# Kernel optimization log

Hardware: AMD Instinct MI355X
Metric: run time of the kernel (lower is better)

## Reference

```python
import jax, jax.numpy as jnp
import numpy as np
from jax import lax

B, N, C = 16, 1024, 768
HID = 128           # route_hidden_dim (Cattn bottleneck + router hidden)
OUT = 2304          # qkv out_feature


def setup_inputs() -> dict:
    key = jax.random.key(0)
    ks = jax.random.split(key, 16)
    s = 0.02
    return {
        "input":  jax.random.normal(ks[0], (B, N, C), jnp.float32),
        "H": 32,
        "W": 32,
        "input2": jax.random.normal(ks[1], (B, N, C), jnp.float32),
        # qkv linear
        "qkv_w": jax.random.normal(ks[2], (OUT, C), jnp.float32) * s,
        "qkv_b": jax.random.normal(ks[3], (OUT,), jnp.float32) * s,
        # Cattn (vida_refine): fc1 -> dwconv -> gelu -> fc2
        "fc1_w": jax.random.normal(ks[4], (HID, C), jnp.float32) * s,
        "fc1_b": jnp.zeros((HID,), jnp.float32),
        "dw_w":  jax.random.normal(ks[5], (HID, 1, 3, 3), jnp.float32) * np.sqrt(2.0 / 9.0),
        "dw_b":  jnp.zeros((HID,), jnp.float32),
        "fc2_w": jax.random.normal(ks[6], (C, HID), jnp.float32) * s,
        "fc2_b": jnp.zeros((C,), jnp.float32),
        # router MLP: 1 -> HID -> 2
        "r1_w": jax.random.normal(ks[7], (HID, 1), jnp.float32) * s,
        "r1_b": jnp.zeros((HID,), jnp.float32),
        "r2_w": jax.random.normal(ks[8], (2, HID), jnp.float32) * s,
        "r2_b": jnp.zeros((2,), jnp.float32),
    }


def _linear(x, w, b):
    return jnp.einsum("bnc,oc->bno", x, w) + b


def _cattn(x, H, W, fc1_w, fc1_b, dw_w, dw_b, fc2_w, fc2_b):
    # fc1 -> depthwise 3x3 conv over HxW -> GELU(exact) -> fc2
    x = _linear(x, fc1_w, fc1_b)                       # [B,N,HID]
    b, n, h = x.shape
    xi = x.transpose(0, 2, 1).reshape(b, h, H, W)      # [B,HID,H,W]
    xi = lax.conv_general_dilated(
        xi, dw_w, window_strides=(1, 1), padding="SAME",
        feature_group_count=h,
        dimension_numbers=("NCHW", "OIHW", "NCHW"),
    ) + dw_b[None, :, None, None]
    x = xi.reshape(b, h, n).transpose(0, 2, 1)         # [B,N,HID]
    x = jax.nn.gelu(x, approximate=False)              # torch nn.GELU default = erf
    return _linear(x, fc2_w, fc2_b)                    # [B,N,C]


def _get_logit(inp, refine_x2):
    # cosine sim between per-batch token-mean of `inp` and refine_x2, then
    # per-batch min-max normalization (skipped when max == min)
    mean = jnp.mean(inp, axis=1, keepdims=True)        # [B,1,C]
    dot = jnp.sum(refine_x2 * mean, axis=-1, keepdims=True)
    n1 = jnp.linalg.norm(mean, axis=-1, keepdims=True)
    n2 = jnp.linalg.norm(refine_x2, axis=-1, keepdims=True)
    csim = dot / (n1 * n2)                             # [B,N,1]
    mn = jnp.min(csim, axis=1, keepdims=True)
    mx = jnp.max(csim, axis=1, keepdims=True)
    rng = mx - mn
    return jnp.where(rng != 0, (csim - mn) / jnp.where(rng != 0, rng, 1.0), csim)


def reference(input, H, W, input2, qkv_w, qkv_b, fc1_w, fc1_b, dw_w, dw_b,
              fc2_w, fc2_b, r1_w, r1_b, r2_w, r2_b):
    q1 = _linear(input, qkv_w, qkv_b)                              # [B,N,OUT]
    refine_x2 = input2 + _cattn(input2, H, W, fc1_w, fc1_b, dw_w, dw_b, fc2_w, fc2_b)
    q2 = _linear(refine_x2, qkv_w, qkv_b)                          # [B,N,OUT]
    csim = _get_logit(input, refine_x2)                            # [B,N,1]
    h = jax.nn.relu(_linear(csim, r1_w, r1_b))                     # [B,N,HID]
    logits = jax.nn.sigmoid(_linear(h, r2_w, r2_b))                # [B,N,2]
    # gumbel_softmax(hard=False, tau=1) with a fixed key for determinism
    g = jax.random.gumbel(jax.random.key(42), logits.shape, logits.dtype)
    router = jax.nn.softmax(logits + g, axis=-1)[:, :, 0]          # [B,N]
    return (q1, q2, router)
```

## Files before the change

kernel.cpp:

```cpp
#include <hip/hip_runtime.h>
#include <cstdint>
#include <cstddef>

#define BQ 16
#define NT 1024
#define CH 768
#define HIDN 128
#define OUTF 2304
#define MTOT (BQ*NT)

typedef __attribute__((ext_vector_type(4))) float f32x4;
typedef __attribute__((ext_vector_type(8))) short short8;

__device__ __forceinline__ unsigned short f2bf(float f){
  unsigned u = __float_as_uint(f);
  u += 0x7FFFu + ((u >> 16) & 1u);
  return (unsigned short)(u >> 16);
}
__device__ __forceinline__ float bf2f(unsigned short h){
  return __uint_as_float(((unsigned)h) << 16);
}

__device__ __forceinline__ void gload16(const void* g, void* l){
  __builtin_amdgcn_global_load_lds((const __attribute__((address_space(1))) void*)g,
                                   (__attribute__((address_space(3))) void*)l, 16, 0, 0);
}

__device__ __forceinline__ void mfma16(f32x4& d, short8 a, short8 b){
  asm volatile("v_mfma_f32_16x16x32_bf16 %0, %1, %2, %0" : "+v"(d) : "v"(a), "v"(b));
}

__global__ void k_f2bf_all(const float* __restrict__ in0, const float* __restrict__ in1,
                           const float* __restrict__ in2, const float* __restrict__ in3,
                           const float* __restrict__ in4,
                           unsigned short* __restrict__ o0, unsigned short* __restrict__ o1,
                           unsigned short* __restrict__ o2, unsigned short* __restrict__ o3,
                           unsigned short* __restrict__ o4)
{
  const long step = (long)2048 * 256 * 4;
  for (long i = (long)(blockIdx.x * 256 + threadIdx.x) * 4; i < 27131904L; i += step){
    const float* s; unsigned short* d; long off;
    if      (i < 12582912L){ s = in0; d = o0; off = i; }
    else if (i < 25165824L){ s = in1; d = o1; off = i - 12582912L; }
    else if (i < 26935296L){ s = in2; d = o2; off = i - 25165824L; }
    else if (i < 27033600L){ s = in3; d = o3; off = i - 26935296L; }
    else                   { s = in4; d = o4; off = i - 27033600L; }
    float4 v = *reinterpret_cast<const float4*>(s + off);
    ushort4 o;
    o.x = f2bf(v.x); o.y = f2bf(v.y); o.z = f2bf(v.z); o.w = f2bf(v.w);
    *reinterpret_cast<ushort4*>(d + off) = o;
  }
}

#define STAGE(matB_, buf_, h_, t_) { \
    const unsigned short* g_ = ((matB_) ? Bbase : Abase) + (size_t)(h_)*128*K + (size_t)(t_)*64; \
    char* d_ = ldsWaveDst + (matB_)*65536 + (buf_)*32768 + (h_)*16384; \
    gload16(g_, d_); \
    gload16(g_ + rowK64, d_ + 8192); \
  }

#define PH_OPEN() \
    asm volatile("s_barrier" ::: "memory"); \
    asm volatile("s_waitcnt lgkmcnt(0)" ::: "memory"); \
    __builtin_amdgcn_sched_barrier(0); \
    __builtin_amdgcn_s_setprio(1);

#define PH_CLOSE() \
    __builtin_amdgcn_s_setprio(0); \
    asm volatile("s_barrier" ::: "memory");

#define MF16(mb, nb, BV) \
    _Pragma("unroll") \
    for (int ks = 0; ks < 2; ++ks) \
      _Pragma("unroll") \
      for (int mf = 0; mf < 4; ++mf) \
        _Pragma("unroll") \
        for (int nf = 0; nf < 2; ++nf) \
          mfma16(acc[(mb)+mf][(nb)+nf], av[mf][ks], BV[nf][ks]);

#define TILE(t_, b_) { \
    const int t = (t_); const int b = (b_); \
    _Pragma("unroll") for (int mf = 0; mf < 4; ++mf){ av[mf][0]=ldA(b,mf,0); av[mf][1]=ldA(b,mf,1); } \
    _Pragma("unroll") for (int nf = 0; nf < 2; ++nf){ b0v[nf][0]=ldB(b,nf,0); b0v[nf][1]=ldB(b,nf,1); } \
    if (t+1 < T) STAGE(0, b^1, 1, t+1); \
    PH_OPEN(); MF16(0,0,b0v); PH_CLOSE(); \
    _Pragma("unroll") for (int nf = 0; nf < 2; ++nf){ b1v[nf][0]=ldB(b,2+nf,0); b1v[nf][1]=ldB(b,2+nf,1); } \
    if (t+1 < T) STAGE(1, b^1, 0, t+1); \
    PH_OPEN(); MF16(0,2,b1v); PH_CLOSE(); \
    _Pragma("unroll") for (int mf = 0; mf < 4; ++mf){ av[mf][0]=ldA(b,4+mf,0); av[mf][1]=ldA(b,4+mf,1); } \
    if (t+2 < T) STAGE(0, b, 0, t+2); \
    PH_OPEN(); MF16(4,2,b1v); PH_CLOSE(); \
    if (t+2 < T) STAGE(1, b, 1, t+2); \
    PH_OPEN(); MF16(4,0,b0v); \
    __builtin_amdgcn_s_setprio(0); \
    if (t+2 < T) { asm volatile("s_waitcnt vmcnt(4)" ::: "memory"); } \
    else         { asm volatile("s_waitcnt vmcnt(0)" ::: "memory"); } \
    asm volatile("s_barrier" ::: "memory"); \
  }

template<int T>
__device__ __forceinline__
void gemm256_body(char* lds8,
                  const unsigned short* __restrict__ A,
                  const unsigned short* __restrict__ B,
                  const float* __restrict__ bias,
                  float* __restrict__ C,
                  int N, int K, int nbn, int bid, int nwg)
{
  const int tid = threadIdx.x;
  const int ln = tid & 63, wv = tid >> 6;
  const int wm = wv >> 2, wn = wv & 3;
  const int llo = ln & 15, lhi = ln >> 4;

  const int cpx = nwg >> 3;
  const int swz = (bid & 7) * cpx + (bid >> 3);
  const int bm = swz / nbn, bn = swz % nbn;
  const int m0 = bm * 256, n0 = bn * 256;

  const int srow = tid >> 3;
  const int sslot = (tid & 7) ^ (srow & 7);
  const unsigned short* Abase = A + (size_t)(m0 + srow) * K + sslot * 8;
  const unsigned short* Bbase = B + (size_t)(n0 + srow) * K + sslot * 8;
  const size_t rowK64 = (size_t)64 * K;
  char* ldsWaveDst = lds8 + (wv << 10);

  const int swz0 = ((lhi ^ (ln & 7)) << 4);
  const char* aRd0 = lds8 + (wm*64 + llo)*128 + swz0;
  const char* aRd1 = lds8 + (wm*64 + llo)*128 + (swz0 ^ 64);
  const char* bRd0 = lds8 + 65536 + (wn*32 + llo)*128 + swz0;
  const char* bRd1 = lds8 + 65536 + (wn*32 + llo)*128 + (swz0 ^ 64);

  auto ldA = [&](int b, int mf, int ks) -> short8 {
    const char* p = (ks ? aRd1 : aRd0) + b*32768 + (mf>>2)*16384 + (mf&3)*2048;
    return *reinterpret_cast<const short8*>(p);
  };
  auto ldB = [&](int b, int nf, int ks) -> short8 {
    const char* p = (ks ? bRd1 : bRd0) + b*32768 + (nf>>1)*16384 + (nf&1)*2048;
    return *reinterpret_cast<const short8*>(p);
  };

  f32x4 acc[8][4];
  #pragma unroll
  for (int m = 0; m < 8; ++m)
    #pragma unroll
    for (int n = 0; n < 4; ++n) acc[m][n] = 0.0f;

  STAGE(0, 0, 0, 0);
  STAGE(1, 0, 1, 0);
  STAGE(0, 0, 1, 0);
  STAGE(1, 0, 0, 0);
  STAGE(0, 1, 0, 1);
  STAGE(1, 1, 1, 1);
  asm volatile("s_waitcnt vmcnt(4)" ::: "memory");
  asm volatile("s_barrier" ::: "memory");

  short8 av[4][2], b0v[2][2], b1v[2][2];
  #pragma unroll 1
  for (int t0 = 0; t0 < T; t0 += 2){
    TILE(t0,   0);
    TILE(t0+1, 1);
  }

  asm volatile("s_nop 7\n\ts_nop 7\n\ts_nop 7" ::: );

  #pragma unroll
  for (int mf = 0; mf < 8; ++mf){
    const int row = m0 + (mf>>2)*128 + wm*64 + (mf&3)*16 + lhi*4;
    #pragma unroll
    for (int j = 0; j < 4; ++j){
      #pragma unroll
      for (int nf = 0; nf < 4; ++nf){
        const int col = n0 + (nf>>1)*128 + wn*32 + (nf&1)*16 + llo;
        C[(size_t)(row + j) * N + col] = acc[mf][nf][j] + bias[col];
      }
    }
  }
}

__device__ __forceinline__
void fc1_body(char* lds, const unsigned short* __restrict__ A,
              const unsigned short* __restrict__ B,
              const float* __restrict__ bias, unsigned short* __restrict__ Cb, int fb)
{
  const int tid = threadIdx.x;
  if (tid >= 256){
    #pragma unroll 1
    for (int i = 0; i < 24; ++i){ __syncthreads(); __syncthreads(); }
    return;
  }
  unsigned short (*sA)[32] = (unsigned short(*)[32])lds;
  unsigned short (*sB)[32] = (unsigned short(*)[32])(lds + 8192);
  const int wv = tid >> 6, ln = tid & 63;
  const int wr = wv >> 1, wc = wv & 1;
  const int lhi = ln >> 4, llo = ln & 15;
  const int m0 = fb * 128, n0 = 0;
  const int N = 128, K = 768;

  f32x4 acc[4][4];
  #pragma unroll
  for (int m = 0; m < 4; ++m)
    #pragma unroll
    for (int n = 0; n < 4; ++n) acc[m][n] = 0.0f;

  const int lrow = ln >> 2;
  const int lk8  = (ln & 3) * 8;

  #pragma unroll 1
  for (int kt = 0; kt < 768; kt += 32){
    #pragma unroll
    for (int cc = 0; cc < 2; ++cc){
      int c = wv * 2 + cc;
      gload16(A + (size_t)(m0 + c*16 + lrow) * K + kt + lk8, &sA[c*16][0]);
      gload16(B + (size_t)(n0 + c*16 + lrow) * K + kt + lk8, &sB[c*16][0]);
    }
    __syncthreads();

    short8 av[4], bv[4];
    #pragma unroll
    for (int m = 0; m < 4; ++m)
      av[m] = *reinterpret_cast<const short8*>(&sA[wr*64 + m*16 + llo][lhi*8]);
    #pragma unroll
    for (int n = 0; n < 4; ++n)
      bv[n] = *reinterpret_cast<const short8*>(&sB[wc*64 + n*16 + llo][lhi*8]);

    #pragma unroll
    for (int m = 0; m < 4; ++m)
      #pragma unroll
      for (int n = 0; n < 4; ++n)
        mfma16(acc[m][n], bv[n], av[m]);
    __syncthreads();
  }

  asm volatile("s_nop 7\n\ts_nop 7\n\ts_nop 7" ::: );

  float4 bias4[4];
  #pragma unroll
  for (int n = 0; n < 4; ++n)
    bias4[n] = *reinterpret_cast<const float4*>(&bias[n0 + wc*64 + n*16 + lhi*4]);

  #pragma unroll
  for (int m = 0; m < 4; ++m){
    const int row = m0 + wr*64 + m*16 + llo;
    #pragma unroll
    for (int n = 0; n < 4; ++n){
      const int colbase = n0 + wc*64 + n*16 + lhi*4;
      ushort4 o;
      o.x = f2bf(acc[m][n][0] + bias4[n].x);
      o.y = f2bf(acc[m][n][1] + bias4[n].y);
      o.z = f2bf(acc[m][n][2] + bias4[n].z);
      o.w = f2bf(acc[m][n][3] + bias4[n].w);
      *reinterpret_cast<ushort4*>(&Cb[(size_t)row * N + colbase]) = o;
    }
  }
}

__device__ __forceinline__
void mean_body(char* lds, const unsigned short* __restrict__ x1b,
               float* __restrict__ meanb, float* __restrict__ n1p, int mbid)
{
  float (*tmp)[128] = (float(*)[128])lds;
  const int b = mbid / 6, cg = mbid % 6;
  const int tid = threadIdx.x;
  const int oct = tid & 15, rg = tid >> 4;
  const unsigned short* ip = x1b + (size_t)b*NT*CH + (size_t)rg*32*CH + cg*128 + oct*8;

  float s[8];
  #pragma unroll
  for (int j = 0; j < 8; ++j) s[j] = 0.f;
  #pragma unroll 4
  for (int r = 0; r < 32; ++r){
    short8 v = *reinterpret_cast<const short8*>(ip + (size_t)r*CH);
    #pragma unroll
    for (int j = 0; j < 8; ++j) s[j] += bf2f((unsigned short)v[j]);
  }
  #pragma unroll
  for (int j = 0; j < 8; ++j) tmp[rg][oct*8 + j] = s[j];
  __syncthreads();

  if (tid < 128){
    float m = 0.f;
    #pragma unroll
    for (int g = 0; g < 32; ++g) m += tmp[g][tid];
    m *= (1.0f/1024.0f);
    meanb[b*CH + cg*128 + tid] = m;
    float q = m * m;
    for (int off = 32; off; off >>= 1) q += __shfl_down(q, off, 64);
    if ((tid & 63) == 0) n1p[b*12 + cg*2 + (tid >> 6)] = q;
  }
}

__global__ __launch_bounds__(512, 2)
void k_combo(const unsigned short* __restrict__ x1b, const unsigned short* __restrict__ wqb,
             const float* __restrict__ qkv_b, float* __restrict__ q1,
             const unsigned short* __restrict__ xrb, const unsigned short* __restrict__ w1b,
             const float* __restrict__ fc1_b, unsigned short* __restrict__ t1dst,
             float* __restrict__ meanb, float* __restrict__ n1p)
{
  __shared__ __align__(1024) char lds8[131072];
  const int bid = blockIdx.x;
  if (bid < 576){
    gemm256_body<CH/64>(lds8, x1b, wqb, qkv_b, q1, OUTF, CH, OUTF/256, bid, 576);
  } else if (bid < 704){
    fc1_body(lds8, xrb, w1b, fc1_b, t1dst, bid - 576);
  } else {
    mean_body(lds8, x1b, meanb, n1p, bid - 704);
  }
}

template<int T>
__global__ __launch_bounds__(512, 2)
void k_gemm256(const unsigned short* __restrict__ A,
               const unsigned short* __restrict__ B,
               const float* __restrict__ bias,
               float* __restrict__ C,
               int N, int K, int nbn)
{
  __shared__ __align__(1024) char lds8[131072];
  gemm256_body<T>(lds8, A, B, bias, C, N, K, nbn, blockIdx.x, gridDim.x);
}

template<int EPI>
__global__ __launch_bounds__(256, 2)
void k_gemm(const unsigned short* __restrict__ A, const unsigned short* __restrict__ B,
            const float* __restrict__ bias, const unsigned short* __restrict__ addb,
            unsigned short* __restrict__ Cb,
            const float* __restrict__ meanb, float* __restrict__ part,
            int M, int N, int K)
{
  __shared__ unsigned short sA[128][32];
  __shared__ unsigned short sB[128][32];
  const int tid = threadIdx.x;
  const int wv = tid >> 6, ln = tid & 63;
  const int wr = wv >> 1, wc = wv & 1;
  const int lhi = ln >> 4, llo = ln & 15;
  const int m0 = blockIdx.x * 128, n0 = blockIdx.y * 128;

  f32x4 acc[4][4];
  #pragma unroll
  for (int m = 0; m < 4; ++m)
    #pragma unroll
    for (int n = 0; n < 4; ++n) acc[m][n] = 0.0f;

  const int lrow = ln >> 2;
  const int lk8  = (ln & 3) * 8;

  for (int kt = 0; kt < K; kt += 32){
    #pragma unroll
    for (int cc = 0; cc < 2; ++cc){
      int c = wv * 2 + cc;
      gload16(A + (size_t)(m0 + c*16 + lrow) * K + kt + lk8, &sA[c*16][0]);
      gload16(B + (size_t)(n0 + c*16 + lrow) * K + kt + lk8, &sB[c*16][0]);
    }
    __syncthreads();

    short8 av[4], bv[4];
    #pragma unroll
    for (int m = 0; m < 4; ++m)
      av[m] = *reinterpret_cast<const short8*>(&sA[wr*64 + m*16 + llo][lhi*8]);
    #pragma unroll
    for (int n = 0; n < 4; ++n)
      bv[n] = *reinterpret_cast<const short8*>(&sB[wc*64 + n*16 + llo][lhi*8]);

    #pragma unroll
    for (int m = 0; m < 4; ++m)
      #pragma unroll
      for (int n = 0; n < 4; ++n)
        mfma16(acc[m][n], bv[n], av[m]);
    __syncthreads();
  }

  asm volatile("s_nop 7\n\ts_nop 7\n\ts_nop 7" ::: );

  float4 bias4[4];
  #pragma unroll
  for (int n = 0; n < 4; ++n)
    bias4[n] = *reinterpret_cast<const float4*>(&bias[n0 + wc*64 + n*16 + lhi*4]);

  {
    const int bb = m0 >> 10;
    const float* mp = meanb + bb * CH;
    float4 mp4[4];
    #pragma unroll
    for (int n = 0; n < 4; ++n)
      mp4[n] = *reinterpret_cast<const float4*>(&mp[n0 + wc*64 + n*16 + lhi*4]);

    #pragma unroll
    for (int m = 0; m < 4; ++m){
      const int row = m0 + wr*64 + m*16 + llo;
      float dsum = 0.f, qsum = 0.f;
      #pragma unroll
      for (int n = 0; n < 4; ++n){
        const int colbase = n0 + wc*64 + n*16 + lhi*4;
        ushort4 a4 = *reinterpret_cast<const ushort4*>(&addb[(size_t)row * N + colbase]);
        float v0 = acc[m][n][0] + bias4[n].x + bf2f(a4.x);
        float v1 = acc[m][n][1] + bias4[n].y + bf2f(a4.y);
        float v2 = acc[m][n][2] + bias4[n].z + bf2f(a4.z);
        float v3 = acc[m][n][3] + bias4[n].w + bf2f(a4.w);
        ushort4 o; o.x = f2bf(v0); o.y = f2bf(v1); o.z = f2bf(v2); o.w = f2bf(v3);
        *reinterpret_cast<ushort4*>(&Cb[(size_t)row * N + colbase]) = o;
        dsum += v0*mp4[n].x + v1*mp4[n].y + v2*mp4[n].z + v3*mp4[n].w;
        qsum += v0*v0 + v1*v1 + v2*v2 + v3*v3;
      }
      dsum += __shfl_xor(dsum, 16, 64);  qsum += __shfl_xor(qsum, 16, 64);
      dsum += __shfl_xor(dsum, 32, 64);  qsum += __shfl_xor(qsum, 32, 64);
      if (ln < 16){
        const int slot = blockIdx.y * 2 + wc;
        part[(size_t)slot * MTOT + row] = dsum;
        part[(size_t)(12 + slot) * MTOT + row] = qsum;
      }
    }
  }
}

__global__ void k_dwgelu(const unsigned short* __restrict__ t1b, const float* __restrict__ dww,
                         const float* __restrict__ dwb, unsigned short* __restrict__ t2)
{
  int idx = blockIdx.x * blockDim.x + threadIdx.x;
  int hq = idx & 31; int t = idx >> 5;
  int h = hq * 4;
  int n = t & (NT-1); int b = t >> 10;
  int y = n >> 5, x = n & 31;

  float w[4][9];
  #pragma unroll
  for (int i = 0; i < 4; ++i)
    #pragma unroll
    for (int k = 0; k < 9; ++k) w[i][k] = dww[(h+i)*9 + k];

  float a0 = dwb[h+0], a1 = dwb[h+1], a2 = dwb[h+2], a3 = dwb[h+3];
  #pragma unroll
  for (int dy = -1; dy <= 1; ++dy){
    int yy = y + dy; if ((unsigned)yy >= 32u) continue;
    #pragma unroll
    for (int dx = -1; dx <= 1; ++dx){
      int xx = x + dx; if ((unsigned)xx >= 32u) continue;
      ushort4 v = *reinterpret_cast<const ushort4*>(&t1b[((size_t)b*NT + yy*32 + xx)*HIDN + h]);
      int k = (dy+1)*3 + (dx+1);
      a0 += bf2f(v.x) * w[0][k]; a1 += bf2f(v.y) * w[1][k];
      a2 += bf2f(v.z) * w[2][k]; a3 += bf2f(v.w) * w[3][k];
    }
  }
  const float is2 = 0.70710678118654752440f;
  a0 = 0.5f*a0*(1.0f + erff(a0*is2));
  a1 = 0.5f*a1*(1.0f + erff(a1*is2));
  a2 = 0.5f*a2*(1.0f + erff(a2*is2));
  a3 = 0.5f*a3*(1.0f + erff(a3*is2));
  ushort4 o; o.x = f2bf(a0); o.y = f2bf(a1); o.z = f2bf(a2); o.w = f2bf(a3);
  *reinterpret_cast<ushort4*>(&t2[(size_t)t*HIDN + h]) = o;
}

__device__ __forceinline__ void threefry(unsigned k0, unsigned k1, unsigned x0, unsigned x1,
                                         unsigned& o0, unsigned& o1){
  unsigned ks2 = k0 ^ k1 ^ 0x1BD11BDAu;
  x0 += k0; x1 += k1;
#define TFR(r) { x0 += x1; x1 = (x1 << r) | (x1 >> (32 - r)); x1 ^= x0; }
  TFR(13) TFR(15) TFR(26) TFR(6)  x0 += k1;  x1 += ks2 + 1u;
  TFR(17) TFR(29) TFR(16) TFR(24) x0 += ks2; x1 += k0 + 2u;
  TFR(13) TFR(15) TFR(26) TFR(6)  x0 += k0;  x1 += k1 + 3u;
  TFR(17) TFR(29) TFR(16) TFR(24) x0 += k1;  x1 += ks2 + 4u;
  TFR(13) TFR(15) TFR(26) TFR(6)  x0 += ks2; x1 += k0 + 5u;
#undef TFR
  o0 = x0; o1 = x1;
}

__device__ __forceinline__ float gumbel_from_bits(unsigned bits){
  float f = __uint_as_float((bits >> 9) | 0x3F800000u) - 1.0f;
  const float TINY = 1.17549435e-38f;
  float u = fmaxf(TINY, f + TINY);
  return -logf(-logf(u));
}

__global__ void k_router(const float* __restrict__ part, const float* __restrict__ n1p,
                         const float* __restrict__ r1w, const float* __restrict__ r1b,
                         const float* __restrict__ r2w, const float* __restrict__ r2b,
                         float* __restrict__ out)
{
  int b = blockIdx.x, tid = threadIdx.x;
  __shared__ float cs[NT];
  __shared__ float red[8];
  __shared__ float w1s[HIDN], b1s[HIDN], w20s[HIDN], w21s[HIDN];
  if (tid < HIDN){
    w1s[tid]  = r1w[tid];
    b1s[tid]  = r1b[tid];
    w20s[tid] = r2w[tid];
    w21s[tid] = r2w[HIDN + tid];
  }
  float n1s = 0.f;
  #pragma unroll
  for (int s = 0; s < 12; ++s) n1s += n1p[b*12 + s];
  float n1 = sqrtf(n1s);
  float lmin = 3.4e38f, lmax = -3.4e38f;
  #pragma unroll
  for (int j = 0; j < 4; ++j){
    int tk = tid + j*256;
    int t = b*NT + tk;
    float dot = 0.f, q = 0.f;
    #pragma unroll
    for (int s = 0; s < 12; ++s){
      dot += part[(size_t)s * MTOT + t];
      q   += part[(size_t)(12 + s) * MTOT + t];
    }
    float v = dot / (n1 * sqrtf(q));
    cs[tk] = v;
    lmin = fminf(lmin, v); lmax = fmaxf(lmax, v);
  }
  int ln = tid & 63, wv = tid >> 6;
  for (int off = 32; off; off >>= 1){
    lmin = fminf(lmin, __shfl_down(lmin, off, 64));
    lmax = fmaxf(lmax, __shfl_down(lmax, off, 64));
  }
  if (ln == 0){ red[wv] = lmin; red[4+wv] = lmax; }
  __syncthreads();
  float mn = fminf(fminf(red[0], red[1]), fminf(red[2], red[3]));
  float mx = fmaxf(fmaxf(red[4], red[5]), fmaxf(red[6], red[7]));
  float rng = mx - mn;
  bool nz = (rng != 0.0f);

  const float r2b0 = r2b[0], r2b1 = r2b[1];
  float v[4], l0[4], l1[4];
  #pragma unroll
  for (int j = 0; j < 4; ++j){
    float c0 = cs[tid + j*256];
    v[j] = nz ? (c0 - mn) / rng : c0;
    l0[j] = r2b0; l1[j] = r2b1;
  }
  for (int k = 0; k < HIDN; ++k){
    float a = w1s[k], bb = b1s[k], c0 = w20s[k], c1 = w21s[k];
    #pragma unroll
    for (int j = 0; j < 4; ++j){
      float hh = fmaxf(v[j] * a + bb, 0.f);
      l0[j] += hh * c0;
      l1[j] += hh * c1;
    }
  }
  #pragma unroll
  for (int j = 0; j < 4; ++j){
    float s0 = 1.f / (1.f + expf(-l0[j]));
    float s1 = 1.f / (1.f + expf(-l1[j]));
    int t = b*NT + tid + j*256;
    unsigned o0, o1;
    threefry(0u, 42u, 0u, (unsigned)(2*t),     o0, o1);
    float g0 = gumbel_from_bits(o0 ^ o1);
    threefry(0u, 42u, 0u, (unsigned)(2*t + 1), o0, o1);
    float g1 = gumbel_from_bits(o0 ^ o1);
    out[t] = 1.f / (1.f + expf((s1 + g1) - (s0 + g0)));
  }
}

extern "C" void kernel_launch(void* const* d_in, const int* in_sizes, int n_in,
                              void* d_out, int out_size, void* d_ws, size_t ws_size,
                              hipStream_t stream)
{
  (void)in_sizes; (void)n_in; (void)out_size;
  const float* input  = (const float*)d_in[0];
  const float* input2 = (const float*)d_in[3];
  const float* qkv_w  = (const float*)d_in[4];
  const float* qkv_b  = (const float*)d_in[5];
  const float* fc1_w  = (const float*)d_in[6];
  const float* fc1_b  = (const float*)d_in[7];
  const float* dw_w   = (const float*)d_in[8];
  const float* dw_b   = (const float*)d_in[9];
  const float* fc2_w  = (const float*)d_in[10];
  const float* fc2_b  = (const float*)d_in[11];
  const float* r1_w   = (const float*)d_in[12];
  const float* r1_b   = (const float*)d_in[13];
  const float* r2_w   = (const float*)d_in[14];
  const float* r2_b   = (const float*)d_in[15];

  float* q1 = (float*)d_out;
  float* q2 = q1 + (size_t)MTOT * OUTF;
  float* router = q1 + (size_t)2 * MTOT * OUTF;

  if (ws_size < 67000000u) return;

  char* ws = (char*)d_ws;
  unsigned short* x1b = (unsigned short*)ws; ws += (size_t)MTOT*CH*2;
  unsigned short* xrb = (unsigned short*)ws; ws += (size_t)MTOT*CH*2;
  unsigned short* wqb = (unsigned short*)ws; ws += (size_t)OUTF*CH*2;
  unsigned short* w1b = (unsigned short*)ws; ws += (size_t)HIDN*CH*2;
  unsigned short* w2b = (unsigned short*)ws; ws += (size_t)CH*HIDN*2;
  unsigned short* t1b = (unsigned short*)ws; ws += (size_t)MTOT*HIDN*4;
  unsigned short* t2  = (unsigned short*)ws; ws += (size_t)MTOT*HIDN*2;
  float*          mb  = (float*)ws;          ws += (size_t)BQ*CH*4;
  float*          n1p = (float*)ws;          ws += 1024;
  float*          part= (float*)t1b;

  k_f2bf_all<<<dim3(2048), 256, 0, stream>>>(
      input, input2, qkv_w, fc1_w, fc2_w, x1b, xrb, wqb, w1b, w2b);

  unsigned short* t1dst = t1b + (size_t)MTOT*HIDN;
  k_combo<<<dim3(800), 512, 0, stream>>>(
      x1b, wqb, qkv_b, q1, xrb, w1b, fc1_b, t1dst, mb, n1p);

  k_dwgelu<<<dim3(MTOT*32/256), 256, 0, stream>>>(t1dst, dw_w, dw_b, t2);

  k_gemm<1><<<dim3(MTOT/128, CH/128), 256, 0, stream>>>(
      t2, w2b, fc2_b, xrb, xrb, mb, part, MTOT, CH, HIDN);

  k_gemm256<CH/64><<<dim3(576), 512, 0, stream>>>(
      xrb, wqb, qkv_b, q2, OUTF, CH, OUTF/256);

  k_router<<<dim3(BQ), 256, 0, stream>>>(part, n1p, r1_w, r1_b, r2_w, r2_b, router);
}
```

Measured before the change: 242.8 us.

## Fold fc2 into q2 GEMM via precomputed Wq·W2 and concatenated K

Rewrites q2 = (x2 + G·W2ᵀ + b2)·Wqᵀ + bq as x2·Wqᵀ + G·(Wq·W2)ᵀ + (bq + Wq·b2). The fused weight and bias are computed in a prep kernel and extra k_combo blocks. The q2 GEMM then runs over a concatenated K of 768+128, and the fc2/cosine-similarity partials are computed in the same launch. This removes the serial dependency of q2 on materializing refine_x2 in bf16 and drops one launch. In exchange it adds about 17% more MFMA work to the q2 GEMM and a serial, poorly coalesced bias-fold kernel, and rounding now differs slightly from the reference order.

```diff
diff --git a/kernel.cpp b/kernel.cpp
--- a/kernel.cpp
+++ b/kernel.cpp
@@ -52,11 +52,41 @@
   }
 }
 
+__global__ void k_prep(const float* __restrict__ qkv_w, const float* __restrict__ qkv_b,
+                       const float* __restrict__ fc2_w, const float* __restrict__ fc2_b,
+                       float* __restrict__ qb2, unsigned short* __restrict__ w2tb,
+                       float* __restrict__ z128)
+{
+  const int bid = blockIdx.x, tid = threadIdx.x;
+  if (bid < 9){
+    __shared__ float fb[CH];
+    for (int i = tid; i < CH; i += 256) fb[i] = fc2_b[i];
+    __syncthreads();
+    int o = bid*256 + tid;
+    float s = qkv_b[o];
+    const float* wr = qkv_w + (size_t)o * CH;
+    for (int c = 0; c < CH; ++c) s += wr[c] * fb[c];
+    qb2[o] = s;
+  } else if (bid < 25){
+    int base = (bid - 9) * 6144;
+    #pragma unroll 4
+    for (int i = 0; i < 24; ++i){
+      int e = base + i*256 + tid;
+      int c = e >> 7, h = e & 127;
+      w2tb[(size_t)h * CH + c] = f2bf(fc2_w[e]);
+    }
+  } else {
+    if (tid < 128) z128[tid] = 0.f;
+  }
+}
+
 #define STAGE(matB_, buf_, h_, t_) { \
-    const unsigned short* g_ = ((matB_) ? Bbase : Abase) + (size_t)(h_)*128*K + (size_t)(t_)*64; \
+    const unsigned short* g_; size_t rk_; \
+    if ((t_) < TS){ g_ = ((matB_) ? Bbase0 : Abase0) + (size_t)(h_)*128*K0 + (size_t)(t_)*64; rk_ = (size_t)64*K0; } \
+    else          { g_ = ((matB_) ? Bbase1 : Abase1) + (size_t)(h_)*128*K1 + (size_t)((t_)-TS)*64; rk_ = (size_t)64*K1; } \
     char* d_ = ldsWaveDst + (matB_)*65536 + (buf_)*32768 + (h_)*16384; \
     gload16(g_, d_); \
-    gload16(g_ + rowK64, d_ + 8192); \
+    gload16(g_ + rk_, d_ + 8192); \
   }
 
 #define PH_OPEN() \
@@ -98,14 +128,14 @@
     asm volatile("s_barrier" ::: "memory"); \
   }
 
-template<int T>
+template<int T, int TS>
 __device__ __forceinline__
 void gemm256_body(char* lds8,
-                  const unsigned short* __restrict__ A,
-                  const unsigned short* __restrict__ B,
+                  const unsigned short* __restrict__ A0, const unsigned short* __restrict__ A1,
+                  const unsigned short* __restrict__ B0, const unsigned short* __restrict__ B1,
                   const float* __restrict__ bias,
                   float* __restrict__ C,
-                  int N, int K, int nbn, int bid, int nwg)
+                  int N, int K0, int K1, int nbn, int bid, int nwg)
 {
   const int tid = threadIdx.x;
   const int ln = tid & 63, wv = tid >> 6;
@@ -119,9 +149,10 @@
 
   const int srow = tid >> 3;
   const int sslot = (tid & 7) ^ (srow & 7);
-  const unsigned short* Abase = A + (size_t)(m0 + srow) * K + sslot * 8;
-  const unsigned short* Bbase = B + (size_t)(n0 + srow) * K + sslot * 8;
-  const size_t rowK64 = (size_t)64 * K;
+  const unsigned short* Abase0 = A0 + (size_t)(m0 + srow) * K0 + sslot * 8;
+  const unsigned short* Abase1 = A1 + (size_t)(m0 + srow) * K1 + sslot * 8;
+  const unsigned short* Bbase0 = B0 + (size_t)(n0 + srow) * K0 + sslot * 8;
+  const unsigned short* Bbase1 = B1 + (size_t)(n0 + srow) * K1 + sslot * 8;
   char* ldsWaveDst = lds8 + (wv << 10);
 
   const int swz0 = ((lhi ^ (ln & 7)) << 4);
@@ -193,7 +224,7 @@
   const int wv = tid >> 6, ln = tid & 63;
   const int wr = wv >> 1, wc = wv & 1;
   const int lhi = ln >> 4, llo = ln & 15;
-  const int m0 = fb * 128, n0 = 0;
+  const int m0 = fb * 128;
   const int N = 128, K = 768;
 
   f32x4 acc[4][4];
@@ -211,7 +242,7 @@
     for (int cc = 0; cc < 2; ++cc){
       int c = wv * 2 + cc;
       gload16(A + (size_t)(m0 + c*16 + lrow) * K + kt + lk8, &sA[c*16][0]);
-      gload16(B + (size_t)(n0 + c*16 + lrow) * K + kt + lk8, &sB[c*16][0]);
+      gload16(B + (size_t)(c*16 + lrow) * K + kt + lk8, &sB[c*16][0]);
     }
     __syncthreads();
 
@@ -236,14 +267,14 @@
   float4 bias4[4];
   #pragma unroll
   for (int n = 0; n < 4; ++n)
-    bias4[n] = *reinterpret_cast<const float4*>(&bias[n0 + wc*64 + n*16 + lhi*4]);
+    bias4[n] = *reinterpret_cast<const float4*>(&bias[wc*64 + n*16 + lhi*4]);
 
   #pragma unroll
   for (int m = 0; m < 4; ++m){
     const int row = m0 + wr*64 + m*16 + llo;
     #pragma unroll
     for (int n = 0; n < 4; ++n){
-      const int colbase = n0 + wc*64 + n*16 + lhi*4;
+      const int colbase = wc*64 + n*16 + lhi*4;
       ushort4 o;
       o.x = f2bf(acc[m][n][0] + bias4[n].x);
       o.y = f2bf(acc[m][n][1] + bias4[n].y);
@@ -255,6 +286,101 @@
 }
 
 __device__ __forceinline__
+void fc2csim_body(char* lds, const unsigned short* __restrict__ A,
+                  const unsigned short* __restrict__ B,
+                  const float* __restrict__ bias, const unsigned short* __restrict__ addb,
+                  const float* __restrict__ meanb, float* __restrict__ part,
+                  int bx, int by)
+{
+  const int tid = threadIdx.x;
+  if (tid >= 256){
+    #pragma unroll 1
+    for (int i = 0; i < 4; ++i){ __syncthreads(); __syncthreads(); }
+    return;
+  }
+  unsigned short (*sA)[32] = (unsigned short(*)[32])lds;
+  unsigned short (*sB)[32] = (unsigned short(*)[32])(lds + 8192);
+  const int wv = tid >> 6, ln = tid & 63;
+  const int wr = wv >> 1, wc = wv & 1;
+  const int lhi = ln >> 4, llo = ln & 15;
+  const int m0 = bx * 128, n0 = by * 128;
+  const int N = CH, K = HIDN;
+
+  f32x4 acc[4][4];
+  #pragma unroll
+  for (int m = 0; m < 4; ++m)
+    #pragma unroll
+    for (int n = 0; n < 4; ++n) acc[m][n] = 0.0f;
+
+  const int lrow = ln >> 2;
+  const int lk8  = (ln & 3) * 8;
+
+  #pragma unroll 1
+  for (int kt = 0; kt < 128; kt += 32){
+    #pragma unroll
+    for (int cc = 0; cc < 2; ++cc){
+      int c = wv * 2 + cc;
+      gload16(A + (size_t)(m0 + c*16 + lrow) * K + kt + lk8, &sA[c*16][0]);
+      gload16(B + (size_t)(n0 + c*16 + lrow) * K + kt + lk8, &sB[c*16][0]);
+    }
+    __syncthreads();
+
+    short8 av[4], bv[4];
+    #pragma unroll
+    for (int m = 0; m < 4; ++m)
+      av[m] = *reinterpret_cast<const short8*>(&sA[wr*64 + m*16 + llo][lhi*8]);
+    #pragma unroll
+    for (int n = 0; n < 4; ++n)
+      bv[n] = *reinterpret_cast<const short8*>(&sB[wc*64 + n*16 + llo][lhi*8]);
+
+    #pragma unroll
+    for (int m = 0; m < 4; ++m)
+      #pragma unroll
+      for (int n = 0; n < 4; ++n)
+        mfma16(acc[m][n], bv[n], av[m]);
+    __syncthreads();
+  }
+
+  asm volatile("s_nop 7\n\ts_nop 7\n\ts_nop 7" ::: );
+
+  float4 bias4[4];
+  #pragma unroll
+  for (int n = 0; n < 4; ++n)
+    bias4[n] = *reinterpret_cast<const float4*>(&bias[n0 + wc*64 + n*16 + lhi*4]);
+
+  const int bb = m0 >> 10;
+  const float* mp = meanb + bb * CH;
+  float4 mp4[4];
+  #pragma unroll
+  for (int n = 0; n < 4; ++n)
+    mp4[n] = *reinterpret_cast<const float4*>(&mp[n0 + wc*64 + n*16 + lhi*4]);
+
+  #pragma unroll
+  for (int m = 0; m < 4; ++m){
+    const int row = m0 + wr*64 + m*16 + llo;
+    float dsum = 0.f, qsum = 0.f;
+    #pragma unroll
+    for (int n = 0; n < 4; ++n){
+      const int colbase = n0 + wc*64 + n*16 + lhi*4;
+      ushort4 a4 = *reinterpret_cast<const ushort4*>(&addb[(size_t)row * N + colbase]);
+      float v0 = acc[m][n][0] + bias4[n].x + bf2f(a4.x);
+      float v1 = acc[m][n][1] + bias4[n].y + bf2f(a4.y);
+      float v2 = acc[m][n][2] + bias4[n].z + bf2f(a4.z);
+      float v3 = acc[m][n][3] + bias4[n].w + bf2f(a4.w);
+      dsum += v0*mp4[n].x + v1*mp4[n].y + v2*mp4[n].z + v3*mp4[n].w;
+      qsum += v0*v0 + v1*v1 + v2*v2 + v3*v3;
+    }
+    dsum += __shfl_xor(dsum, 16, 64);  qsum += __shfl_xor(qsum, 16, 64);
+    dsum += __shfl_xor(dsum, 32, 64);  qsum += __shfl_xor(qsum, 32, 64);
+    if (ln < 16){
+      const int slot = by * 2 + wc;
+      part[(size_t)slot * MTOT + row] = dsum;
+      part[(size_t)(12 + slot) * MTOT + row] = qsum;
+    }
+  }
+}
+
+__device__ __forceinline__
 void mean_body(char* lds, const unsigned short* __restrict__ x1b,
                float* __restrict__ meanb, float* __restrict__ n1p, int mbid)
 {
@@ -292,123 +418,41 @@
 __global__ __launch_bounds__(512, 2)
 void k_combo(const unsigned short* __restrict__ x1b, const unsigned short* __restrict__ wqb,
              const float* __restrict__ qkv_b, float* __restrict__ q1,
-             const unsigned short* __restrict__ xrb, const unsigned short* __restrict__ w1b,
+             const unsigned short* __restrict__ x2b, const unsigned short* __restrict__ w1b,
              const float* __restrict__ fc1_b, unsigned short* __restrict__ t1dst,
-             float* __restrict__ meanb, float* __restrict__ n1p)
+             float* __restrict__ meanb, float* __restrict__ n1p,
+             const unsigned short* __restrict__ w2tb, const float* __restrict__ z128,
+             unsigned short* __restrict__ W2q)
 {
   __shared__ __align__(1024) char lds8[131072];
   const int bid = blockIdx.x;
   if (bid < 576){
-    gemm256_body<CH/64>(lds8, x1b, wqb, qkv_b, q1, OUTF, CH, OUTF/256, bid, 576);
+    gemm256_body<CH/64, CH/64>(lds8, x1b, x1b, wqb, wqb, qkv_b, q1,
+                               OUTF, CH, CH, OUTF/256, bid, 576);
   } else if (bid < 704){
-    fc1_body(lds8, xrb, w1b, fc1_b, t1dst, bid - 576);
+    fc1_body(lds8, x2b, w1b, fc1_b, t1dst, bid - 576);
+  } else if (bid < 800){
+    mean_body(lds8, x1b, meanb, n1p, bid - 704);
   } else {
-    mean_body(lds8, x1b, meanb, n1p, bid - 704);
-  }
-}
-
-template<int T>
+    fc1_body(lds8, wqb, w2tb, z128, W2q, bid - 800);
+  }
+}
+
 __global__ __launch_bounds__(512, 2)
-void k_gemm256(const unsigned short* __restrict__ A,
-               const unsigned short* __restrict__ B,
-               const float* __restrict__ bias,
-               float* __restrict__ C,
-               int N, int K, int nbn)
+void k_combo2(const unsigned short* __restrict__ x2b, const unsigned short* __restrict__ G,
+              const unsigned short* __restrict__ wqb, const unsigned short* __restrict__ W2q,
+              const float* __restrict__ qb2, float* __restrict__ q2,
+              const unsigned short* __restrict__ w2b, const float* __restrict__ fc2_b,
+              const float* __restrict__ meanb, float* __restrict__ part)
 {
   __shared__ __align__(1024) char lds8[131072];
-  gemm256_body<T>(lds8, A, B, bias, C, N, K, nbn, blockIdx.x, gridDim.x);
-}
-
-template<int EPI>
-__global__ __launch_bounds__(256, 2)
-void k_gemm(const unsigned short* __restrict__ A, const unsigned short* __restrict__ B,
-            const float* __restrict__ bias, const unsigned short* __restrict__ addb,
-            unsigned short* __restrict__ Cb,
-            const float* __restrict__ meanb, float* __restrict__ part,
-            int M, int N, int K)
-{
-  __shared__ unsigned short sA[128][32];
-  __shared__ unsigned short sB[128][32];
-  const int tid = threadIdx.x;
-  const int wv = tid >> 6, ln = tid & 63;
-  const int wr = wv >> 1, wc = wv & 1;
-  const int lhi = ln >> 4, llo = ln & 15;
-  const int m0 = blockIdx.x * 128, n0 = blockIdx.y * 128;
-
-  f32x4 acc[4][4];
-  #pragma unroll
-  for (int m = 0; m < 4; ++m)
-    #pragma unroll
-    for (int n = 0; n < 4; ++n) acc[m][n] = 0.0f;
-
-  const int lrow = ln >> 2;
-  const int lk8  = (ln & 3) * 8;
-
-  for (int kt = 0; kt < K; kt += 32){
-    #pragma unroll
-    for (int cc = 0; cc < 2; ++cc){
-      int c = wv * 2 + cc;
-      gload16(A + (size_t)(m0 + c*16 + lrow) * K + kt + lk8, &sA[c*16][0]);
-      gload16(B + (size_t)(n0 + c*16 + lrow) * K + kt + lk8, &sB[c*16][0]);
-    }
-    __syncthreads();
-
-    short8 av[4], bv[4];
-    #pragma unroll
-    for (int m = 0; m < 4; ++m)
-      av[m] = *reinterpret_cast<const short8*>(&sA[wr*64 + m*16 + llo][lhi*8]);
-    #pragma unroll
-    for (int n = 0; n < 4; ++n)
-      bv[n] = *reinterpret_cast<const short8*>(&sB[wc*64 + n*16 + llo][lhi*8]);
-
-    #pragma unroll
-    for (int m = 0; m < 4; ++m)
-      #pragma unroll
-      for (int n = 0; n < 4; ++n)
-        mfma16(acc[m][n], bv[n], av[m]);
-    __syncthreads();
-  }
-
-  asm volatile("s_nop 7\n\ts_nop 7\n\ts_nop 7" ::: );
-
-  float4 bias4[4];
-  #pragma unroll
-  for (int n = 0; n < 4; ++n)
-    bias4[n] = *reinterpret_cast<const float4*>(&bias[n0 + wc*64 + n*16 + lhi*4]);
-
-  {
-    const int bb = m0 >> 10;
-    const float* mp = meanb + bb * CH;
-    float4 mp4[4];
-    #pragma unroll
-    for (int n = 0; n < 4; ++n)
-      mp4[n] = *reinterpret_cast<const float4*>(&mp[n0 + wc*64 + n*16 + lhi*4]);
-
-    #pragma unroll
-    for (int m = 0; m < 4; ++m){
-      const int row = m0 + wr*64 + m*16 + llo;
-      float dsum = 0.f, qsum = 0.f;
-      #pragma unroll
-      for (int n = 0; n < 4; ++n){
-        const int colbase = n0 + wc*64 + n*16 + lhi*4;
-        ushort4 a4 = *reinterpret_cast<const ushort4*>(&addb[(size_t)row * N + colbase]);
-        float v0 = acc[m][n][0] + bias4[n].x + bf2f(a4.x);
-        float v1 = acc[m][n][1] + bias4[n].y + bf2f(a4.y);
-        float v2 = acc[m][n][2] + bias4[n].z + bf2f(a4.z);
-        float v3 = acc[m][n][3] + bias4[n].w + bf2f(a4.w);
-        ushort4 o; o.x = f2bf(v0); o.y = f2bf(v1); o.z = f2bf(v2); o.w = f2bf(v3);
-        *reinterpret_cast<ushort4*>(&Cb[(size_t)row * N + colbase]) = o;
-        dsum += v0*mp4[n].x + v1*mp4[n].y + v2*mp4[n].z + v3*mp4[n].w;
-        qsum += v0*v0 + v1*v1 + v2*v2 + v3*v3;
-      }
-      dsum += __shfl_xor(dsum, 16, 64);  qsum += __shfl_xor(qsum, 16, 64);
-      dsum += __shfl_xor(dsum, 32, 64);  qsum += __shfl_xor(qsum, 32, 64);
-      if (ln < 16){
-        const int slot = blockIdx.y * 2 + wc;
-        part[(size_t)slot * MTOT + row] = dsum;
-        part[(size_t)(12 + slot) * MTOT + row] = qsum;
-      }
-    }
+  const int bid = blockIdx.x;
+  if (bid < 576){
+    gemm256_body<14, 12>(lds8, x2b, G, wqb, W2q, qb2, q2,
+                         OUTF, CH, HIDN, OUTF/256, bid, 576);
+  } else {
+    const int idx = bid - 576;
+    fc2csim_body(lds8, G, w2b, fc2_b, x2b, meanb, part, idx / 6, idx % 6);
   }
 }
 
@@ -575,30 +619,34 @@
 
   char* ws = (char*)d_ws;
   unsigned short* x1b = (unsigned short*)ws; ws += (size_t)MTOT*CH*2;
-  unsigned short* xrb = (unsigned short*)ws; ws += (size_t)MTOT*CH*2;
+  unsigned short* x2b = (unsigned short*)ws; ws += (size_t)MTOT*CH*2;
   unsigned short* wqb = (unsigned short*)ws; ws += (size_t)OUTF*CH*2;
   unsigned short* w1b = (unsigned short*)ws; ws += (size_t)HIDN*CH*2;
   unsigned short* w2b = (unsigned short*)ws; ws += (size_t)CH*HIDN*2;
-  unsigned short* t1b = (unsigned short*)ws; ws += (size_t)MTOT*HIDN*4;
+  char*           reg = ws;                  ws += (size_t)MTOT*HIDN*4;
   unsigned short* t2  = (unsigned short*)ws; ws += (size_t)MTOT*HIDN*2;
   float*          mb  = (float*)ws;          ws += (size_t)BQ*CH*4;
   float*          n1p = (float*)ws;          ws += 1024;
-  float*          part= (float*)t1b;
+
+  float*          part  = (float*)reg;
+  unsigned short* w2tb  = (unsigned short*)(reg + 1572864);
+  unsigned short* W2q   = (unsigned short*)(reg + 1769472);
+  float*          qb2   = (float*)(reg + 2359296);
+  float*          z128  = (float*)(reg + 2368512);
+  unsigned short* t1dst = (unsigned short*)(reg + 4194304);
 
   k_f2bf_all<<<dim3(2048), 256, 0, stream>>>(
-      input, input2, qkv_w, fc1_w, fc2_w, x1b, xrb, wqb, w1b, w2b);
-
-  unsigned short* t1dst = t1b + (size_t)MTOT*HIDN;
-  k_combo<<<dim3(800), 512, 0, stream>>>(
-      x1b, wqb, qkv_b, q1, xrb, w1b, fc1_b, t1dst, mb, n1p);
+      input, input2, qkv_w, fc1_w, fc2_w, x1b, x2b, wqb, w1b, w2b);
+
+  k_prep<<<dim3(26), 256, 0, stream>>>(qkv_w, qkv_b, fc2_w, fc2_b, qb2, w2tb, z128);
+
+  k_combo<<<dim3(818), 512, 0, stream>>>(
+      x1b, wqb, qkv_b, q1, x2b, w1b, fc1_b, t1dst, mb, n1p, w2tb, z128, W2q);
 
   k_dwgelu<<<dim3(MTOT*32/256), 256, 0, stream>>>(t1dst, dw_w, dw_b, t2);
 
-  k_gemm<1><<<dim3(MTOT/128, CH/128), 256, 0, stream>>>(
-      t2, w2b, fc2_b, xrb, xrb, mb, part, MTOT, CH, HIDN);
-
-  k_gemm256<CH/64><<<dim3(576), 512, 0, stream>>>(
-      xrb, wqb, qkv_b, q2, OUTF, CH, OUTF/256);
+  k_combo2<<<dim3(1344), 512, 0, stream>>>(
+      x2b, t2, wqb, W2q, qb2, q2, w2b, fc2_b, mb, part);
 
   k_router<<<dim3(BQ), 256, 0, stream>>>(part, n1p, r1_w, r1_b, r2_w, r2_b, router);
 }
```

Measured after the change: 267.9 us. 1.1x slower.
